# Performance work log

Hardware: AMD Instinct MI355X
Metric: run time of the kernel (lower is better)

Reference implementation:

```python
import jax, jax.numpy as jnp
import numpy as np

N = 10000   # num_nodes
F = 64      # latent_dim
U = 128     # num_units
B = 8       # batch
K = 2       # gcn_step
E = 160000  # edges (avg degree 16)
M = 2 * K + 1  # num_matrices = len(supports)*gcn_step + 1


def setup_inputs() -> dict:
    rng = np.random.default_rng(0)
    rows = rng.integers(0, N, E).astype(np.int32)
    cols = rng.integers(0, N, E).astype(np.int32)
    vals = (rng.random(E).astype(np.float32) + 0.1)
    # random-walk normalization D^{-1} A, per the original utils.calculate_random_walk_matrix
    deg_out = np.zeros(N, np.float32); np.add.at(deg_out, rows, vals)
    deg_in = np.zeros(N, np.float32); np.add.at(deg_in, cols, vals)
    # support1 = (D_out^{-1} A)^T : out[c] += vals/d_out[r] * x[r]  -> dst=cols, src=rows
    w1 = vals / np.maximum(deg_out[rows], 1e-8)
    # support2 = (D_in^{-1} A^T)^T : out[r] += vals/d_in[c] * x[c]  -> dst=rows, src=cols
    w2 = vals / np.maximum(deg_in[cols], 1e-8)

    key = jax.random.key(0)
    ks = jax.random.split(key, 4)

    def xavier(k, shape):
        std = (2.0 / (shape[0] + shape[1])) ** 0.5
        return jax.random.normal(k, shape, jnp.float32) * std

    return {
        'y': jax.random.normal(ks[0], (B, N * F), jnp.float32),
        'W_lat': xavier(ks[1], (M * F, F)),
        'b_lat': jnp.ones((F,), jnp.float32),   # bias_start=1.0, shared (keyed by length)
        'W_units': xavier(ks[2], (M * F, U)),
        'b_units': jnp.zeros((U,), jnp.float32),
        'W_final': xavier(ks[3], (M * U, F)),
        'sup1_w': jnp.asarray(w1),
        'sup2_w': jnp.asarray(w2),
        'edge_rows': jnp.asarray(rows),
        'edge_cols': jnp.asarray(cols),
    }


def _spmm(dst, src, w, x):
    # sparse matmul S @ x with S given as COO edge list; x: (N, Fin, B)
    return jax.ops.segment_sum(w[:, None, None] * x[src], dst, num_segments=N)


def _gconv(x, supports, W, b):
    # x: (B, N, Fin) -> (B, N*Fout); Chebyshev diffusion convolution
    Bsz, n, fin = x.shape
    x0 = jnp.transpose(x, (1, 2, 0))  # (N, Fin, B)
    xs = [x0]
    for dst, src, w in supports:
        xk_2 = x0
        x1 = _spmm(dst, src, w, x0)
        xs.append(x1)
        for _ in range(2, K + 1):
            x2 = 2.0 * _spmm(dst, src, w, x1) - xk_2
            xs.append(x2)
            xk_2, x1 = x1, x2
    X = jnp.stack(xs, axis=-1)                       # (N, Fin, B, M)
    X = jnp.transpose(X, (2, 0, 1, 3)).reshape(Bsz * n, fin * len(xs))  # feature-major, matrix-minor
    out = X @ W + b
    return out.reshape(Bsz, n * W.shape[1])


def reference(y, W_lat, b_lat, W_units, b_units, W_final, sup1_w, sup2_w, edge_rows, edge_cols):
    supports = [(edge_cols, edge_rows, sup1_w), (edge_rows, edge_cols, sup2_w)]
    x = y.reshape(B, N, F)
    # theta gate (bias_start=1.0 via shared b_lat)
    theta = jax.nn.sigmoid(_gconv(x, supports, W_lat, b_lat))
    # ode_func_net: gen_layers=1 hidden gconv + final gconv (final bias is shared b_lat!)
    c = jnp.tanh(_gconv(x, supports, W_units, b_units)).reshape(B, N, U)
    c = jnp.tanh(_gconv(c, supports, W_final, b_lat))
    return -theta * c
```

## Files before the change

### kernel.cpp

```cpp
#include <hip/hip_runtime.h>

#define N_NODES 10000
#define NEDGE 160000
#define NB 80000

typedef unsigned int u32;
typedef unsigned short u16;
typedef __attribute__((ext_vector_type(8))) short short8;
typedef __attribute__((ext_vector_type(4))) float float4v;

__device__ __forceinline__ u16 f2bf(float f) {
    u32 u = __float_as_uint(f);
    return (u16)((u + 0x7fffu + ((u >> 16) & 1u)) >> 16);
}
__device__ __forceinline__ float lo16(u32 u) { return __uint_as_float(u << 16); }
__device__ __forceinline__ float hi16(u32 u) { return __uint_as_float(u & 0xffff0000u); }
__device__ __forceinline__ u32 pack2(float a, float b) {
    return (u32)f2bf(a) | (((u32)f2bf(b)) << 16);
}
__device__ __forceinline__ float fast_tanh(float v) {
    return 1.f - 2.f / (__expf(2.f * v) + 1.f);
}

static const size_t SLAB = (size_t)NB * 64;

__global__ __launch_bounds__(256) void prepcount_kernel(
    const float2* __restrict__ y, u32* __restrict__ X0,
    const float* __restrict__ W_lat, const float* __restrict__ W_units,
    u16* __restrict__ bpk12, const float* __restrict__ W_final, u16* __restrict__ bpkP,
    const int* __restrict__ rows, const int* __restrict__ cols, int* __restrict__ cnt) {
    int b = blockIdx.x, t = threadIdx.x;
    if (b < 10000) {
        int idx = b * 256 + t;
        int fh = idx & 31;
        int rb = idx >> 5;
        int bb = rb & 7;
        int n = rb >> 3;
        float2 v = y[((size_t)bb * N_NODES + n) * 32 + fh];
        X0[idx] = pack2(v.x, v.y);
    } else if (b < 10240) {
        int idx = (b - 10000) * 256 + t;
        int j = idx & 7;
        int lane = (idx >> 3) & 63;
        int rest = idx >> 9;
        int ct = rest % 12;
        int ks = rest / 12;
        int k = ks * 32 + (lane >> 4) * 8 + j;
        int col = ct * 16 + (lane & 15);
        int wrow = (k % 64) * 5 + (k / 64);
        float v = (col < 64) ? W_lat[wrow * 64 + col] : W_units[wrow * 128 + (col - 64)];
        bpk12[idx] = f2bf(v);
    } else if (b < 10400) {
        int idx = (b - 10240) * 256 + t;
        int j8 = idx & 7;
        int lane = (idx >> 3) & 63;
        int rest = idx >> 9;
        int ct = rest % 20;
        int ks = rest / 20;
        int k = ks * 32 + (lane >> 4) * 8 + j8;
        int col = ct * 16 + (lane & 15);
        int slot = col >> 6, j = col & 63;
        float v;
        if (slot == 0)
            v = W_final[(k * 5 + 0) * 64 + j] - W_final[(k * 5 + 2) * 64 + j] -
                W_final[(k * 5 + 4) * 64 + j];
        else
            v = W_final[(k * 5 + slot) * 64 + j];
        bpkP[idx] = f2bf(v);
    } else {
        int e = (b - 10400) * 256 + t;
        atomicAdd(&cnt[cols[e]], 1);
        atomicAdd(&cnt[N_NODES + rows[e]], 1);
    }
}

__global__ void blocksum_kernel(const int* __restrict__ cnt, int* __restrict__ bsums) {
    __shared__ int red[4];
    int arr = blockIdx.x / 40;
    int c = blockIdx.x % 40;
    int idx = c * 256 + threadIdx.x;
    int v = (idx < N_NODES) ? cnt[arr * N_NODES + idx] : 0;
#pragma unroll
    for (int off = 32; off; off >>= 1) v += __shfl_down(v, off, 64);
    int wv = threadIdx.x >> 6, ln = threadIdx.x & 63;
    if (ln == 0) red[wv] = v;
    __syncthreads();
    if (threadIdx.x == 0) bsums[blockIdx.x] = red[0] + red[1] + red[2] + red[3];
}

__global__ void scanapply_kernel(int* __restrict__ cnt, const int* __restrict__ bsums,
                                 int* __restrict__ rowptr1, int* __restrict__ rowptr2) {
    __shared__ int lds[256];
    int arr = blockIdx.x / 40;
    int c = blockIdx.x % 40;
    int base = 0;
    for (int i = 0; i < c; i++) base += bsums[arr * 40 + i];
    int idx = c * 256 + threadIdx.x;
    bool ok = idx < N_NODES;
    int v = ok ? cnt[arr * N_NODES + idx] : 0;
    int t = threadIdx.x;
    lds[t] = v;
    __syncthreads();
    for (int off = 1; off < 256; off <<= 1) {
        int add = (t >= off) ? lds[t - off] : 0;
        __syncthreads();
        lds[t] += add;
        __syncthreads();
    }
    int excl = lds[t] - v + base;
    if (ok) {
        int* rp = arr ? rowptr2 : rowptr1;
        rp[idx] = excl;
        cnt[arr * N_NODES + idx] = excl;
    }
    if (blockIdx.x == 0 && t == 0) {
        rowptr1[N_NODES] = NEDGE;
        rowptr2[N_NODES] = NEDGE;
    }
}

__global__ void scatter_kernel(const int* __restrict__ rows, const int* __restrict__ cols,
                               const float* __restrict__ w1, const float* __restrict__ w2,
                               int* __restrict__ cur1, int* __restrict__ cur2,
                               int2* __restrict__ edges1, int2* __restrict__ edges2) {
    int e = blockIdx.x * 256 + threadIdx.x;
    if (e < NEDGE) {
        int r = rows[e], c = cols[e];
        int p1 = atomicAdd(&cur1[c], 1);
        edges1[p1] = make_int2(r, __float_as_int(w1[e]));
        int p2 = atomicAdd(&cur2[r], 1);
        edges2[p2] = make_int2(c, __float_as_int(w2[e]));
    }
}

__device__ __forceinline__ void gacc(float* acc, float w, uint4 u) {
    acc[0] += w * lo16(u.x); acc[1] += w * hi16(u.x);
    acc[2] += w * lo16(u.y); acc[3] += w * hi16(u.y);
    acc[4] += w * lo16(u.z); acc[5] += w * hi16(u.z);
    acc[6] += w * lo16(u.w); acc[7] += w * hi16(u.w);
}

__device__ __forceinline__ void gather_row(const u32* __restrict__ Xin,
                                           const int* __restrict__ rp,
                                           const int2* __restrict__ eg,
                                           int n, int lane, float* acc) {
    int e0 = rp[n], e1 = rp[n + 1];
    for (int base = e0; base < e1; base += 64) {
        int m = min(64, e1 - base);
        int2 me = make_int2(0, 0);
        if (lane < m) me = eg[base + lane];
        int j = 0;
        for (; j + 4 <= m; j += 4) {
            int s0 = __shfl(me.x, j, 64);
            int s1 = __shfl(me.x, j + 1, 64);
            int s2 = __shfl(me.x, j + 2, 64);
            int s3 = __shfl(me.x, j + 3, 64);
            float w0 = __int_as_float(__shfl(me.y, j, 64));
            float w1 = __int_as_float(__shfl(me.y, j + 1, 64));
            float w2 = __int_as_float(__shfl(me.y, j + 2, 64));
            float w3 = __int_as_float(__shfl(me.y, j + 3, 64));
            uint4 u0 = *(const uint4*)(Xin + (size_t)s0 * 256 + lane * 4);
            uint4 u1 = *(const uint4*)(Xin + (size_t)s1 * 256 + lane * 4);
            uint4 u2 = *(const uint4*)(Xin + (size_t)s2 * 256 + lane * 4);
            uint4 u3 = *(const uint4*)(Xin + (size_t)s3 * 256 + lane * 4);
            gacc(acc, w0, u0);
            gacc(acc, w1, u1);
            gacc(acc, w2, u2);
            gacc(acc, w3, u3);
        }
        for (; j < m; j++) {
            int src = __shfl(me.x, j, 64);
            float w = __int_as_float(__shfl(me.y, j, 64));
            uint4 u = *(const uint4*)(Xin + (size_t)src * 256 + lane * 4);
            gacc(acc, w, u);
        }
    }
}

__global__ __launch_bounds__(256) void spmm2_kernel(
    const u32* __restrict__ XinA, const u32* __restrict__ XprevA, u32* __restrict__ XoutA,
    const u32* __restrict__ XinB, const u32* __restrict__ XprevB, u32* __restrict__ XoutB,
    const int* __restrict__ rowptr1, const int2* __restrict__ edges1,
    const int* __restrict__ rowptr2, const int2* __restrict__ edges2,
    float alpha, float beta) {
    int lane = threadIdx.x & 63;
    int v = blockIdx.x * 4 + (threadIdx.x >> 6);
    if (v >= 2 * N_NODES) return;
    bool hB = v >= N_NODES;
    int n = hB ? v - N_NODES : v;
    const u32* Xin = hB ? XinB : XinA;
    const u32* Xprev = hB ? XprevB : XprevA;
    u32* Xout = hB ? XoutB : XoutA;
    const int* rp = hB ? rowptr2 : rowptr1;
    const int2* eg = hB ? edges2 : edges1;

    float acc[8] = {0.f, 0.f, 0.f, 0.f, 0.f, 0.f, 0.f, 0.f};
    gather_row(Xin, rp, eg, n, lane, acc);

    size_t o = (size_t)n * 256 + lane * 4;
    if (beta != 0.f) {
        uint4 p = *(const uint4*)(Xprev + o);
        acc[0] = alpha * acc[0] + beta * lo16(p.x); acc[1] = alpha * acc[1] + beta * hi16(p.x);
        acc[2] = alpha * acc[2] + beta * lo16(p.y); acc[3] = alpha * acc[3] + beta * hi16(p.y);
        acc[4] = alpha * acc[4] + beta * lo16(p.z); acc[5] = alpha * acc[5] + beta * hi16(p.z);
        acc[6] = alpha * acc[6] + beta * lo16(p.w); acc[7] = alpha * acc[7] + beta * hi16(p.w);
    } else {
#pragma unroll
        for (int i = 0; i < 8; i++) acc[i] *= alpha;
    }
    uint4 r;
    r.x = pack2(acc[0], acc[1]);
    r.y = pack2(acc[2], acc[3]);
    r.z = pack2(acc[4], acc[5]);
    r.w = pack2(acc[6], acc[7]);
    *(uint4*)(Xout + o) = r;
}

__global__ __launch_bounds__(256) void spmm_final_kernel(
    const u32* __restrict__ T1, const u32* __restrict__ T2,
    const u32* __restrict__ Q, const u32* __restrict__ theta,
    const int* __restrict__ rowptr1, const int2* __restrict__ edges1,
    const int* __restrict__ rowptr2, const int2* __restrict__ edges2,
    float* __restrict__ outF) {
    int lane = threadIdx.x & 63;
    int n = blockIdx.x * 4 + (threadIdx.x >> 6);
    if (n >= N_NODES) return;

    float acc[8] = {0.f, 0.f, 0.f, 0.f, 0.f, 0.f, 0.f, 0.f};
    gather_row(T1, rowptr1, edges1, n, lane, acc);
    gather_row(T2, rowptr2, edges2, n, lane, acc);

    size_t o = (size_t)n * 256 + lane * 4;
    uint4 q = *(const uint4*)(Q + o);
    uint4 th = *(const uint4*)(theta + o);
    float res[8];
    res[0] = -lo16(th.x) * fast_tanh(lo16(q.x) + acc[0]);
    res[1] = -hi16(th.x) * fast_tanh(hi16(q.x) + acc[1]);
    res[2] = -lo16(th.y) * fast_tanh(lo16(q.y) + acc[2]);
    res[3] = -hi16(th.y) * fast_tanh(hi16(q.y) + acc[3]);
    res[4] = -lo16(th.z) * fast_tanh(lo16(q.z) + acc[4]);
    res[5] = -hi16(th.z) * fast_tanh(hi16(q.z) + acc[5]);
    res[6] = -lo16(th.w) * fast_tanh(lo16(q.w) + acc[6]);
    res[7] = -hi16(th.w) * fast_tanh(hi16(q.w) + acc[7]);
    int b = lane >> 3;
    int f0 = ((lane * 4) & 31) * 2;
    float* dst = outF + (size_t)b * (N_NODES * 64) + (size_t)n * 64 + f0;
    *(float4*)(dst) = make_float4(res[0], res[1], res[2], res[3]);
    *(float4*)(dst + 4) = make_float4(res[4], res[5], res[6], res[7]);
}

struct Slabs { const u16* p[5]; };

template <int FIN, int NM, int NOUT, int NSPLIT, int MODE>
__global__ __launch_bounds__(256) void gemm_kernel(
    Slabs A, const u16* __restrict__ Bp, const float* __restrict__ bias1,
    const float* __restrict__ bias2, u16* __restrict__ O1, u16* __restrict__ O2) {
    constexpr int K = NM * FIN;
    constexpr int KS = K / 32;
    constexpr int CTT = NOUT / 16;
    constexpr int CT = CTT / NSPLIT;
    int lane = threadIdx.x & 63;
    int wave = threadIdx.x >> 6;
    int rowBase = (blockIdx.x / NSPLIT) * 64 + wave * 16;
    int ctBase = (blockIdx.x % NSPLIT) * CT;
    int mrow = lane & 15;
    int kq = lane >> 4;

    float4v acc[CT];
#pragma unroll
    for (int c = 0; c < CT; c++) acc[c] = (float4v){0.f, 0.f, 0.f, 0.f};

#pragma unroll
    for (int ks = 0; ks < KS; ks++) {
        int k = ks * 32 + kq * 8;
        int m = k / FIN;
        int koff = k % FIN;
        short8 a = *(const short8*)(A.p[m] + (size_t)(rowBase + mrow) * FIN + koff);
        short8 b[CT];
#pragma unroll
        for (int ct = 0; ct < CT; ct++)
            b[ct] = *(const short8*)(Bp + ((size_t)(ks * CTT + ctBase + ct) * 64 + lane) * 8);
#pragma unroll
        for (int ct = 0; ct < CT; ct++)
            acc[ct] = __builtin_amdgcn_mfma_f32_16x16x32_bf16(a, b[ct], acc[ct], 0, 0, 0);
    }

    int rowq = rowBase + kq * 4;
#pragma unroll
    for (int ct = 0; ct < CT; ct++) {
        int col = (ctBase + ct) * 16 + mrow;
        float bsv;
        if (MODE == 0) bsv = (col < 64) ? bias1[col] : 0.f;
        else bsv = (col < 64) ? bias1[col] : bias2[col - 64];
#pragma unroll
        for (int i = 0; i < 4; i++) {
            float v = acc[ct][i] + bsv;
            int r = rowq + i;
            if (MODE == 0) {
                O1[(size_t)(col >> 6) * SLAB + (size_t)r * 64 + (col & 63)] = f2bf(v);
            } else {
                if (col < 64) {
                    v = 1.f / (1.f + __expf(-v));
                    O1[(size_t)r * 64 + col] = f2bf(v);
                } else {
                    O2[(size_t)r * 128 + (col - 64)] = f2bf(fast_tanh(v));
                }
            }
        }
    }
}

extern "C" void kernel_launch(void* const* d_in, const int* in_sizes, int n_in,
                              void* d_out, int out_size, void* d_ws, size_t ws_size,
                              hipStream_t stream) {
    const float2* y    = (const float2*)d_in[0];
    const float* W_lat = (const float*)d_in[1];
    const float* b_lat = (const float*)d_in[2];
    const float* W_units = (const float*)d_in[3];
    const float* b_units = (const float*)d_in[4];
    const float* W_final = (const float*)d_in[5];
    const float* sup1w = (const float*)d_in[6];
    const float* sup2w = (const float*)d_in[7];
    const int* rows    = (const int*)d_in[8];
    const int* cols    = (const int*)d_in[9];
    float* out = (float*)d_out;

    char* ws = (char*)d_ws;
    size_t off = 0;
    auto alloc = [&](size_t bytes) -> void* {
        void* p = ws + off;
        off += (bytes + 511) & ~(size_t)511;
        return p;
    };
    int* rowptr1 = (int*)alloc((N_NODES + 1) * 4);
    int* rowptr2 = (int*)alloc((N_NODES + 1) * 4);
    int* cnt = (int*)alloc((size_t)2 * N_NODES * 4);
    int* bsums = (int*)alloc(80 * 4);
    int2* edges1 = (int2*)alloc((size_t)NEDGE * 8);
    int2* edges2 = (int2*)alloc((size_t)NEDGE * 8);
    u16* bpk12 = (u16*)alloc((size_t)61440 * 2);
    u16* bpkP = (u16*)alloc((size_t)40960 * 2);
    u16* theta = (u16*)alloc((size_t)NB * 64 * 2);
    u16* S = (u16*)alloc((size_t)5 * NB * 64 * 2);
    u16* H0 = (u16*)alloc((size_t)NB * 128 * 2);
    u16* T1 = (u16*)alloc((size_t)NB * 64 * 2);
    u16* T2 = (u16*)alloc((size_t)NB * 64 * 2);

    hipMemsetAsync(cnt, 0, (size_t)2 * N_NODES * 4, stream);
    prepcount_kernel<<<11025, 256, 0, stream>>>(y, (u32*)S, W_lat, W_units, bpk12,
                                                W_final, bpkP, rows, cols, cnt);
    blocksum_kernel<<<80, 256, 0, stream>>>(cnt, bsums);
    scanapply_kernel<<<80, 256, 0, stream>>>(cnt, bsums, rowptr1, rowptr2);
    scatter_kernel<<<625, 256, 0, stream>>>(rows, cols, sup1w, sup2w,
                                            cnt, cnt + N_NODES, edges1, edges2);

    const u32* S0 = (const u32*)S;
    u32* X1 = (u32*)(S + 1 * SLAB);
    u32* X2 = (u32*)(S + 2 * SLAB);
    u32* X3 = (u32*)(S + 3 * SLAB);
    u32* X4 = (u32*)(S + 4 * SLAB);
    spmm2_kernel<<<5000, 256, 0, stream>>>(S0, nullptr, X1, S0, nullptr, X3,
                                           rowptr1, edges1, rowptr2, edges2, 1.f, 0.f);
    spmm2_kernel<<<5000, 256, 0, stream>>>(X1, S0, X2, X3, S0, X4,
                                           rowptr1, edges1, rowptr2, edges2, 2.f, -1.f);

    Slabs SX;
    for (int m = 0; m < 5; m++) SX.p[m] = S + (size_t)m * SLAB;
    gemm_kernel<64, 5, 192, 1, 1><<<1250, 256, 0, stream>>>(SX, bpk12, b_lat, b_units, theta, H0);

    Slabs SH;
    SH.p[0] = H0;
    gemm_kernel<128, 1, 320, 2, 0><<<2500, 256, 0, stream>>>(SH, bpkP, b_lat, nullptr, S, nullptr);

    const u32* Q  = (const u32*)(S + 0 * SLAB);
    const u32* P1 = (const u32*)(S + 1 * SLAB);
    const u32* P2 = (const u32*)(S + 2 * SLAB);
    const u32* P3 = (const u32*)(S + 3 * SLAB);
    const u32* P4 = (const u32*)(S + 4 * SLAB);
    spmm2_kernel<<<5000, 256, 0, stream>>>(P2, P1, (u32*)T1, P4, P3, (u32*)T2,
                                           rowptr1, edges1, rowptr2, edges2, 2.f, 1.f);
    spmm_final_kernel<<<2500, 256, 0, stream>>>((const u32*)T1, (const u32*)T2, Q,
                                                (const u32*)theta,
                                                rowptr1, edges1, rowptr2, edges2, out);
}
```

Measured before the change: 348.8 us.

## Pad CSR rows to multiples of eight and gather with readlane-unrolled batches

```diff
diff --git a/kernel.cpp b/kernel.cpp
--- a/kernel.cpp
+++ b/kernel.cpp
@@ -3,6 +3,7 @@
 #define N_NODES 10000
 #define NEDGE 160000
 #define NB 80000
+#define EPAD (NEDGE + 8 * N_NODES)
 
 typedef unsigned int u32;
 typedef unsigned short u16;
@@ -79,7 +80,7 @@
     int arr = blockIdx.x / 40;
     int c = blockIdx.x % 40;
     int idx = c * 256 + threadIdx.x;
-    int v = (idx < N_NODES) ? cnt[arr * N_NODES + idx] : 0;
+    int v = (idx < N_NODES) ? ((cnt[arr * N_NODES + idx] + 7) & ~7) : 0;
 #pragma unroll
     for (int off = 32; off; off >>= 1) v += __shfl_down(v, off, 64);
     int wv = threadIdx.x >> 6, ln = threadIdx.x & 63;
@@ -97,7 +98,7 @@
     for (int i = 0; i < c; i++) base += bsums[arr * 40 + i];
     int idx = c * 256 + threadIdx.x;
     bool ok = idx < N_NODES;
-    int v = ok ? cnt[arr * N_NODES + idx] : 0;
+    int v = ok ? ((cnt[arr * N_NODES + idx] + 7) & ~7) : 0;
     int t = threadIdx.x;
     lds[t] = v;
     __syncthreads();
@@ -113,9 +114,8 @@
         rp[idx] = excl;
         cnt[arr * N_NODES + idx] = excl;
     }
-    if (blockIdx.x == 0 && t == 0) {
-        rowptr1[N_NODES] = NEDGE;
-        rowptr2[N_NODES] = NEDGE;
+    if (c == 39 && t == 255) {
+        (arr ? rowptr2 : rowptr1)[N_NODES] = base + lds[255];
     }
 }
 
@@ -140,40 +140,60 @@
     acc[6] += w * lo16(u.w); acc[7] += w * hi16(u.w);
 }
 
+#define G8(J)                                                                   \
+    if (m > (J)) {                                                              \
+        int s0 = __builtin_amdgcn_readlane(me.x, (J) + 0);                      \
+        int s1 = __builtin_amdgcn_readlane(me.x, (J) + 1);                      \
+        int s2 = __builtin_amdgcn_readlane(me.x, (J) + 2);                      \
+        int s3 = __builtin_amdgcn_readlane(me.x, (J) + 3);                      \
+        int s4 = __builtin_amdgcn_readlane(me.x, (J) + 4);                      \
+        int s5 = __builtin_amdgcn_readlane(me.x, (J) + 5);                      \
+        int s6 = __builtin_amdgcn_readlane(me.x, (J) + 6);                      \
+        int s7 = __builtin_amdgcn_readlane(me.x, (J) + 7);                      \
+        uint4 u0 = *(const uint4*)(Xin + (size_t)s0 * 256 + lane4);             \
+        uint4 u1 = *(const uint4*)(Xin + (size_t)s1 * 256 + lane4);             \
+        uint4 u2 = *(const uint4*)(Xin + (size_t)s2 * 256 + lane4);             \
+        uint4 u3 = *(const uint4*)(Xin + (size_t)s3 * 256 + lane4);             \
+        uint4 u4 = *(const uint4*)(Xin + (size_t)s4 * 256 + lane4);             \
+        uint4 u5 = *(const uint4*)(Xin + (size_t)s5 * 256 + lane4);             \
+        uint4 u6 = *(const uint4*)(Xin + (size_t)s6 * 256 + lane4);             \
+        uint4 u7 = *(const uint4*)(Xin + (size_t)s7 * 256 + lane4);             \
+        float w0 = __int_as_float(__builtin_amdgcn_readlane(me.y, (J) + 0));    \
+        float w1 = __int_as_float(__builtin_amdgcn_readlane(me.y, (J) + 1));    \
+        float w2 = __int_as_float(__builtin_amdgcn_readlane(me.y, (J) + 2));    \
+        float w3 = __int_as_float(__builtin_amdgcn_readlane(me.y, (J) + 3));    \
+        float w4 = __int_as_float(__builtin_amdgcn_readlane(me.y, (J) + 4));    \
+        float w5 = __int_as_float(__builtin_amdgcn_readlane(me.y, (J) + 5));    \
+        float w6 = __int_as_float(__builtin_amdgcn_readlane(me.y, (J) + 6));    \
+        float w7 = __int_as_float(__builtin_amdgcn_readlane(me.y, (J) + 7));    \
+        gacc(acc, w0, u0);                                                      \
+        gacc(acc, w1, u1);                                                      \
+        gacc(acc, w2, u2);                                                      \
+        gacc(acc, w3, u3);                                                      \
+        gacc(acc, w4, u4);                                                      \
+        gacc(acc, w5, u5);                                                      \
+        gacc(acc, w6, u6);                                                      \
+        gacc(acc, w7, u7);                                                      \
+    }
+
 __device__ __forceinline__ void gather_row(const u32* __restrict__ Xin,
                                            const int* __restrict__ rp,
                                            const int2* __restrict__ eg,
                                            int n, int lane, float* acc) {
     int e0 = rp[n], e1 = rp[n + 1];
+    int lane4 = lane * 4;
     for (int base = e0; base < e1; base += 64) {
         int m = min(64, e1 - base);
         int2 me = make_int2(0, 0);
         if (lane < m) me = eg[base + lane];
-        int j = 0;
-        for (; j + 4 <= m; j += 4) {
-            int s0 = __shfl(me.x, j, 64);
-            int s1 = __shfl(me.x, j + 1, 64);
-            int s2 = __shfl(me.x, j + 2, 64);
-            int s3 = __shfl(me.x, j + 3, 64);
-            float w0 = __int_as_float(__shfl(me.y, j, 64));
-            float w1 = __int_as_float(__shfl(me.y, j + 1, 64));
-            float w2 = __int_as_float(__shfl(me.y, j + 2, 64));
-            float w3 = __int_as_float(__shfl(me.y, j + 3, 64));
-            uint4 u0 = *(const uint4*)(Xin + (size_t)s0 * 256 + lane * 4);
-            uint4 u1 = *(const uint4*)(Xin + (size_t)s1 * 256 + lane * 4);
-            uint4 u2 = *(const uint4*)(Xin + (size_t)s2 * 256 + lane * 4);
-            uint4 u3 = *(const uint4*)(Xin + (size_t)s3 * 256 + lane * 4);
-            gacc(acc, w0, u0);
-            gacc(acc, w1, u1);
-            gacc(acc, w2, u2);
-            gacc(acc, w3, u3);
-        }
-        for (; j < m; j++) {
-            int src = __shfl(me.x, j, 64);
-            float w = __int_as_float(__shfl(me.y, j, 64));
-            uint4 u = *(const uint4*)(Xin + (size_t)src * 256 + lane * 4);
-            gacc(acc, w, u);
-        }
+        G8(0)
+        G8(8)
+        G8(16)
+        G8(24)
+        G8(32)
+        G8(40)
+        G8(48)
+        G8(56)
     }
 }
 
@@ -336,8 +356,8 @@
     int* rowptr2 = (int*)alloc((N_NODES + 1) * 4);
     int* cnt = (int*)alloc((size_t)2 * N_NODES * 4);
     int* bsums = (int*)alloc(80 * 4);
-    int2* edges1 = (int2*)alloc((size_t)NEDGE * 8);
-    int2* edges2 = (int2*)alloc((size_t)NEDGE * 8);
+    int2* edges1 = (int2*)alloc((size_t)EPAD * 8);
+    int2* edges2 = (int2*)alloc((size_t)EPAD * 8);
     u16* bpk12 = (u16*)alloc((size_t)61440 * 2);
     u16* bpkP = (u16*)alloc((size_t)40960 * 2);
     u16* theta = (u16*)alloc((size_t)NB * 64 * 2);
@@ -347,6 +367,8 @@
     u16* T2 = (u16*)alloc((size_t)NB * 64 * 2);
 
     hipMemsetAsync(cnt, 0, (size_t)2 * N_NODES * 4, stream);
+    hipMemsetAsync(edges1, 0, (size_t)EPAD * 8, stream);
+    hipMemsetAsync(edges2, 0, (size_t)EPAD * 8, stream);
     prepcount_kernel<<<11025, 256, 0, stream>>>(y, (u32*)S, W_lat, W_units, bpk12,
                                                 W_final, bpkP, rows, cols, cnt);
     blocksum_kernel<<<80, 256, 0, stream>>>(cnt, bsums);
```

New measurement: 351.6 us. No clear change (+0.8%).

## Pad CSR rows to multiples of eight and gather with 8-lane groups per row

Applied to the files above, without the earlier changes.

```diff
diff --git a/kernel.cpp b/kernel.cpp
--- a/kernel.cpp
+++ b/kernel.cpp
@@ -3,6 +3,7 @@
 #define N_NODES 10000
 #define NEDGE 160000
 #define NB 80000
+#define EPAD (NEDGE + 8 * N_NODES)
 
 typedef unsigned int u32;
 typedef unsigned short u16;
@@ -79,7 +80,7 @@
     int arr = blockIdx.x / 40;
     int c = blockIdx.x % 40;
     int idx = c * 256 + threadIdx.x;
-    int v = (idx < N_NODES) ? cnt[arr * N_NODES + idx] : 0;
+    int v = (idx < N_NODES) ? ((cnt[arr * N_NODES + idx] + 7) & ~7) : 0;
 #pragma unroll
     for (int off = 32; off; off >>= 1) v += __shfl_down(v, off, 64);
     int wv = threadIdx.x >> 6, ln = threadIdx.x & 63;
@@ -97,7 +98,7 @@
     for (int i = 0; i < c; i++) base += bsums[arr * 40 + i];
     int idx = c * 256 + threadIdx.x;
     bool ok = idx < N_NODES;
-    int v = ok ? cnt[arr * N_NODES + idx] : 0;
+    int v = ok ? ((cnt[arr * N_NODES + idx] + 7) & ~7) : 0;
     int t = threadIdx.x;
     lds[t] = v;
     __syncthreads();
@@ -113,9 +114,8 @@
         rp[idx] = excl;
         cnt[arr * N_NODES + idx] = excl;
     }
-    if (blockIdx.x == 0 && t == 0) {
-        rowptr1[N_NODES] = NEDGE;
-        rowptr2[N_NODES] = NEDGE;
+    if (c == 39 && t == 255) {
+        (arr ? rowptr2 : rowptr1)[N_NODES] = base + lds[255];
     }
 }
 
@@ -140,40 +140,27 @@
     acc[6] += w * lo16(u.w); acc[7] += w * hi16(u.w);
 }
 
-__device__ __forceinline__ void gather_row(const u32* __restrict__ Xin,
-                                           const int* __restrict__ rp,
-                                           const int2* __restrict__ eg,
-                                           int n, int lane, float* acc) {
-    int e0 = rp[n], e1 = rp[n + 1];
-    for (int base = e0; base < e1; base += 64) {
-        int m = min(64, e1 - base);
+__device__ __forceinline__ void gather_sliced(const u32* __restrict__ Xin,
+                                              const int* __restrict__ rp,
+                                              const int2* __restrict__ eg,
+                                              int row, bool valid, int su, int l,
+                                              float* acc) {
+    int e = 0, e1 = 0;
+    if (valid) {
+        e = rp[row] + l;
+        e1 = rp[row + 1];
+    }
+    while (__ballot(e < e1)) {
         int2 me = make_int2(0, 0);
-        if (lane < m) me = eg[base + lane];
-        int j = 0;
-        for (; j + 4 <= m; j += 4) {
-            int s0 = __shfl(me.x, j, 64);
-            int s1 = __shfl(me.x, j + 1, 64);
-            int s2 = __shfl(me.x, j + 2, 64);
-            int s3 = __shfl(me.x, j + 3, 64);
-            float w0 = __int_as_float(__shfl(me.y, j, 64));
-            float w1 = __int_as_float(__shfl(me.y, j + 1, 64));
-            float w2 = __int_as_float(__shfl(me.y, j + 2, 64));
-            float w3 = __int_as_float(__shfl(me.y, j + 3, 64));
-            uint4 u0 = *(const uint4*)(Xin + (size_t)s0 * 256 + lane * 4);
-            uint4 u1 = *(const uint4*)(Xin + (size_t)s1 * 256 + lane * 4);
-            uint4 u2 = *(const uint4*)(Xin + (size_t)s2 * 256 + lane * 4);
-            uint4 u3 = *(const uint4*)(Xin + (size_t)s3 * 256 + lane * 4);
-            gacc(acc, w0, u0);
-            gacc(acc, w1, u1);
-            gacc(acc, w2, u2);
-            gacc(acc, w3, u3);
-        }
-        for (; j < m; j++) {
-            int src = __shfl(me.x, j, 64);
-            float w = __int_as_float(__shfl(me.y, j, 64));
-            uint4 u = *(const uint4*)(Xin + (size_t)src * 256 + lane * 4);
+        if (e < e1) me = eg[e];
+#pragma unroll
+        for (int j = 0; j < 8; j++) {
+            int s = __shfl(me.x, j, 8);
+            float w = __int_as_float(__shfl(me.y, j, 8));
+            uint4 u = *(const uint4*)(Xin + (size_t)s * 256 + su + l * 4);
             gacc(acc, w, u);
         }
+        e += 8;
     }
 }
 
@@ -183,9 +170,13 @@
     const int* __restrict__ rowptr1, const int2* __restrict__ edges1,
     const int* __restrict__ rowptr2, const int2* __restrict__ edges2,
     float alpha, float beta) {
-    int lane = threadIdx.x & 63;
-    int v = blockIdx.x * 4 + (threadIdx.x >> 6);
-    if (v >= 2 * N_NODES) return;
+    int t = threadIdx.x;
+    int lane = t & 63;
+    int g = lane >> 3, l = lane & 7;
+    int slice = blockIdx.x & 7;
+    int chunk = blockIdx.x >> 3;
+    int su = slice * 32;
+    int v = chunk * 32 + (t >> 6) * 8 + g;
     bool hB = v >= N_NODES;
     int n = hB ? v - N_NODES : v;
     const u32* Xin = hB ? XinB : XinA;
@@ -195,9 +186,9 @@
     const int2* eg = hB ? edges2 : edges1;
 
     float acc[8] = {0.f, 0.f, 0.f, 0.f, 0.f, 0.f, 0.f, 0.f};
-    gather_row(Xin, rp, eg, n, lane, acc);
-
-    size_t o = (size_t)n * 256 + lane * 4;
+    gather_sliced(Xin, rp, eg, n, true, su, l, acc);
+
+    size_t o = (size_t)n * 256 + su + l * 4;
     if (beta != 0.f) {
         uint4 p = *(const uint4*)(Xprev + o);
         acc[0] = alpha * acc[0] + beta * lo16(p.x); acc[1] = alpha * acc[1] + beta * hi16(p.x);
@@ -222,15 +213,21 @@
     const int* __restrict__ rowptr1, const int2* __restrict__ edges1,
     const int* __restrict__ rowptr2, const int2* __restrict__ edges2,
     float* __restrict__ outF) {
-    int lane = threadIdx.x & 63;
-    int n = blockIdx.x * 4 + (threadIdx.x >> 6);
-    if (n >= N_NODES) return;
+    int t = threadIdx.x;
+    int lane = t & 63;
+    int g = lane >> 3, l = lane & 7;
+    int slice = blockIdx.x & 7;
+    int chunk = blockIdx.x >> 3;
+    int su = slice * 32;
+    int n = chunk * 32 + (t >> 6) * 8 + g;
+    bool valid = n < N_NODES;
 
     float acc[8] = {0.f, 0.f, 0.f, 0.f, 0.f, 0.f, 0.f, 0.f};
-    gather_row(T1, rowptr1, edges1, n, lane, acc);
-    gather_row(T2, rowptr2, edges2, n, lane, acc);
-
-    size_t o = (size_t)n * 256 + lane * 4;
+    gather_sliced(T1, rowptr1, edges1, n, valid, su, l, acc);
+    gather_sliced(T2, rowptr2, edges2, n, valid, su, l, acc);
+    if (!valid) return;
+
+    size_t o = (size_t)n * 256 + su + l * 4;
     uint4 q = *(const uint4*)(Q + o);
     uint4 th = *(const uint4*)(theta + o);
     float res[8];
@@ -242,9 +239,7 @@
     res[5] = -hi16(th.z) * fast_tanh(hi16(q.z) + acc[5]);
     res[6] = -lo16(th.w) * fast_tanh(lo16(q.w) + acc[6]);
     res[7] = -hi16(th.w) * fast_tanh(hi16(q.w) + acc[7]);
-    int b = lane >> 3;
-    int f0 = ((lane * 4) & 31) * 2;
-    float* dst = outF + (size_t)b * (N_NODES * 64) + (size_t)n * 64 + f0;
+    float* dst = outF + (size_t)slice * (N_NODES * 64) + (size_t)n * 64 + l * 8;
     *(float4*)(dst) = make_float4(res[0], res[1], res[2], res[3]);
     *(float4*)(dst + 4) = make_float4(res[4], res[5], res[6], res[7]);
 }
@@ -336,8 +331,8 @@
     int* rowptr2 = (int*)alloc((N_NODES + 1) * 4);
     int* cnt = (int*)alloc((size_t)2 * N_NODES * 4);
     int* bsums = (int*)alloc(80 * 4);
-    int2* edges1 = (int2*)alloc((size_t)NEDGE * 8);
-    int2* edges2 = (int2*)alloc((size_t)NEDGE * 8);
+    int2* edges1 = (int2*)alloc((size_t)EPAD * 8);
+    int2* edges2 = (int2*)alloc((size_t)EPAD * 8);
     u16* bpk12 = (u16*)alloc((size_t)61440 * 2);
     u16* bpkP = (u16*)alloc((size_t)40960 * 2);
     u16* theta = (u16*)alloc((size_t)NB * 64 * 2);
@@ -347,6 +342,8 @@
     u16* T2 = (u16*)alloc((size_t)NB * 64 * 2);
 
     hipMemsetAsync(cnt, 0, (size_t)2 * N_NODES * 4, stream);
+    hipMemsetAsync(edges1, 0, (size_t)EPAD * 8, stream);
+    hipMemsetAsync(edges2, 0, (size_t)EPAD * 8, stream);
     prepcount_kernel<<<11025, 256, 0, stream>>>(y, (u32*)S, W_lat, W_units, bpk12,
                                                 W_final, bpkP, rows, cols, cnt);
     blocksum_kernel<<<80, 256, 0, stream>>>(cnt, bsums);
@@ -379,7 +376,7 @@
     const u32* P4 = (const u32*)(S + 4 * SLAB);
     spmm2_kernel<<<5000, 256, 0, stream>>>(P2, P1, (u32*)T1, P4, P3, (u32*)T2,
                                            rowptr1, edges1, rowptr2, edges2, 2.f, 1.f);
-    spmm_final_kernel<<<2500, 256, 0, stream>>>((const u32*)T1, (const u32*)T2, Q,
+    spmm_final_kernel<<<2504, 256, 0, stream>>>((const u32*)T1, (const u32*)T2, Q,
                                                 (const u32*)theta,
                                                 rowptr1, edges1, rowptr2, edges2, out);
 }
```

After: 314.1 us. 9.9% less time.
